# Performance work log

Hardware: AMD Instinct MI355X
Metric: run time of the kernel (lower is better)

## Reference

```python
import jax, jax.numpy as jnp
import numpy as np

B, S, DIM, DA = 64, 4096, 256, 64
NEG = -1e30

def setup_inputs() -> dict:
    key = jax.random.key(0)
    k1, k2, k3, k4 = jax.random.split(key, 4)
    h = jax.random.normal(k1, (B, S, DIM), dtype=jnp.float32)
    mask = jax.random.randint(k2, (B, S), 0, 2).astype(jnp.bool_)
    # xavier_uniform with gain=1.414 as in the torch module
    lim_a = 1.414 * np.sqrt(6.0 / (DIM + DA))
    lim_b = 1.414 * np.sqrt(6.0 / (DA + 1))
    a = jax.random.uniform(k3, (DIM, DA), minval=-lim_a, maxval=lim_a, dtype=jnp.float32)
    b = jax.random.uniform(k4, (DA, 1), minval=-lim_b, maxval=lim_b, dtype=jnp.float32)
    return {"h": h, "mask": mask, "a": a, "b": b}

def reference(h, mask, a, b):
    # e: (B, S) additive-attention logits
    e = jnp.einsum('bsk,ko->bs', jnp.tanh(jnp.einsum('bsd,dk->bsk', h, a)), b)
    e = e + mask.astype(e.dtype) * NEG  # True == padding -> -1e30
    attn = jax.nn.softmax(e, axis=1)    # softmax over seq dim
    # weighted sum over seq: (B, DIM)
    return jnp.einsum('bs,bsd->bd', attn, h)
```

## Files before the change

### kernel.cpp

```cpp
#include <hip/hip_runtime.h>
#include <hip/hip_bf16.h>

#define B_      64
#define S_      4096
#define DIM_    256
#define DA_     64
#define NEG_    (-1e30f)
#define CHUNKS_ 16
#define ROWS_   256
#define TILES_  4
#define LDH_    264
#define PSTR_   258

typedef _Float16 half8 __attribute__((ext_vector_type(8)));
typedef float float4v __attribute__((ext_vector_type(4)));

__global__ __launch_bounds__(256) void prep_kernel(
    const float* __restrict__ a, const void* __restrict__ mask,
    _Float16* __restrict__ at_sw, int* __restrict__ flag)
{
    int idx = blockIdx.x * 256 + threadIdx.x;
    int j    = idx & 7;
    int lane = (idx >> 3) & 63;
    int kbnt = idx >> 9;
    int kb   = kbnt & 7;
    int nt   = kbnt >> 3;
    int d  = kb * 32 + (lane >> 4) * 8 + j;
    int kf = nt * 16 + (lane & 15);
    at_sw[idx] = (_Float16)a[d * DA_ + kf];

    if (blockIdx.x == 0) {
        __shared__ int anynz;
        if (threadIdx.x == 0) anynz = 0;
        __syncthreads();
        const unsigned char* mb = (const unsigned char*)mask;
        int base = threadIdx.x * 4;
        int v = mb[base + 1] | mb[base + 2] | mb[base + 3];
        if (v) atomicOr(&anynz, 1);
        __syncthreads();
        if (threadIdx.x == 0) *flag = (anynz == 0) ? 1 : 0;
    }
}

__global__ __launch_bounds__(256) void fused_kernel(
    const float* __restrict__ h, const _Float16* __restrict__ at_sw,
    const float* __restrict__ bvec, const void* __restrict__ mask,
    const int* __restrict__ flag, float* __restrict__ part)
{
    __shared__ _Float16 hf[64 * LDH_];
    __shared__ float e_l[64];
    __shared__ float w_l[64];
    __shared__ float red[4 * 256];
    __shared__ float m_s, l_s, resc_s;

    const int t = threadIdx.x;
    const int b = blockIdx.x >> 4;
    const int c = blockIdx.x & (CHUNKS_ - 1);
    const int wave = t >> 6;
    const int lane = t & 63;
    const int quad = lane >> 4;
    const int nrow = lane & 15;
    const bool int32enc = (*flag != 0);

    if (t == 0) { m_s = NEG_; l_s = 0.f; }

    const float* hb = h + ((long long)b * S_ + c * ROWS_) * DIM_;
    float bv[4];
    #pragma unroll
    for (int nt = 0; nt < 4; ++nt) bv[nt] = bvec[nt * 16 + nrow];

    const int dbase = (t & 63) * 4;
    float acc0 = 0.f, acc1 = 0.f, acc2 = 0.f, acc3 = 0.f;

    for (int tile = 0; tile < TILES_; ++tile) {
        const float* hsrc = hb + (size_t)tile * 64 * DIM_;
        #pragma unroll
        for (int j = 0; j < 8; ++j) {
            int f2 = t + j * 256;
            int row = f2 >> 5;
            int col = (f2 & 31) * 8;
            const float* src = hsrc + row * DIM_ + col;
            float4 v0 = *(const float4*)(src);
            float4 v1 = *(const float4*)(src + 4);
            union { _Float16 hh[8]; uint4 u; } pk;
            pk.hh[0] = (_Float16)v0.x; pk.hh[1] = (_Float16)v0.y;
            pk.hh[2] = (_Float16)v0.z; pk.hh[3] = (_Float16)v0.w;
            pk.hh[4] = (_Float16)v1.x; pk.hh[5] = (_Float16)v1.y;
            pk.hh[6] = (_Float16)v1.z; pk.hh[7] = (_Float16)v1.w;
            *(uint4*)&hf[row * LDH_ + col] = pk.u;
        }
        __syncthreads();

        float4v accm[4];
        #pragma unroll
        for (int nt = 0; nt < 4; ++nt) accm[nt] = (float4v){0.f, 0.f, 0.f, 0.f};
        const _Float16* hrow = &hf[(wave * 16 + nrow) * LDH_];
        #pragma unroll
        for (int kb = 0; kb < 8; ++kb) {
            half8 af = *(const half8*)(hrow + kb * 32 + quad * 8);
            #pragma unroll
            for (int nt = 0; nt < 4; ++nt) {
                half8 bf = *(const half8*)(at_sw + ((nt * 8 + kb) * 64 + lane) * 8);
                accm[nt] = __builtin_amdgcn_mfma_f32_16x16x32_f16(af, bf, accm[nt], 0, 0, 0);
            }
        }
        #pragma unroll
        for (int r = 0; r < 4; ++r) {
            float p = 0.f;
            #pragma unroll
            for (int nt = 0; nt < 4; ++nt) p += tanhf(accm[nt][r]) * bv[nt];
            p += __shfl_xor(p, 1);
            p += __shfl_xor(p, 2);
            p += __shfl_xor(p, 4);
            p += __shfl_xor(p, 8);
            if (nrow == r) e_l[wave * 16 + quad * 4 + r] = p;
        }
        __syncthreads();

        if (wave == 0) {
            long long mi = (long long)b * S_ + c * ROWS_ + tile * 64 + lane;
            int mv = int32enc ? ((const int*)mask)[mi]
                              : (int)((const unsigned char*)mask)[mi];
            float ev = mv ? NEG_ : e_l[lane];
            float mx = ev;
            #pragma unroll
            for (int off = 32; off >= 1; off >>= 1) mx = fmaxf(mx, __shfl_xor(mx, off));
            float m_old = m_s;
            float m_new = fmaxf(m_old, mx);
            float wv_ = __expf(ev - m_new);
            w_l[lane] = wv_;
            float sm = wv_;
            #pragma unroll
            for (int off = 32; off >= 1; off >>= 1) sm += __shfl_xor(sm, off);
            if (lane == 0) {
                float rs = __expf(m_old - m_new);
                l_s = l_s * rs + sm;
                m_s = m_new;
                resc_s = rs;
            }
        }
        __syncthreads();

        float rs = resc_s;
        acc0 *= rs; acc1 *= rs; acc2 *= rs; acc3 *= rs;
        #pragma unroll 4
        for (int i = 0; i < 16; ++i) {
            int s = i * 4 + wave;
            float ws = w_l[s];
            union { ushort4 u; _Float16 hh[4]; } pk;
            pk.u = *(const ushort4*)((const unsigned short*)&hf[s * LDH_ + dbase]);
            acc0 = fmaf(ws, (float)pk.hh[0], acc0);
            acc1 = fmaf(ws, (float)pk.hh[1], acc1);
            acc2 = fmaf(ws, (float)pk.hh[2], acc2);
            acc3 = fmaf(ws, (float)pk.hh[3], acc3);
        }
        __syncthreads();
    }

    red[wave * 256 + dbase + 0] = acc0;
    red[wave * 256 + dbase + 1] = acc1;
    red[wave * 256 + dbase + 2] = acc2;
    red[wave * 256 + dbase + 3] = acc3;
    __syncthreads();
    float sum = red[t] + red[256 + t] + red[512 + t] + red[768 + t];
    float* pc = part + (size_t)(b * CHUNKS_ + c) * PSTR_;
    pc[2 + t] = sum;
    if (t == 0) { pc[0] = m_s; pc[1] = l_s; }
}

__global__ __launch_bounds__(256) void merge_kernel(
    const float* __restrict__ part, float* __restrict__ out)
{
    const int b = blockIdx.x;
    const int t = threadIdx.x;
    const float* pb = part + (size_t)b * CHUNKS_ * PSTR_;
    float M = NEG_;
    #pragma unroll
    for (int c = 0; c < CHUNKS_; ++c) M = fmaxf(M, pb[c * PSTR_]);
    float L = 0.f, o = 0.f;
    #pragma unroll
    for (int c = 0; c < CHUNKS_; ++c) {
        float sc = __expf(pb[c * PSTR_] - M);
        L += pb[c * PSTR_ + 1] * sc;
        o += pb[c * PSTR_ + 2 + t] * sc;
    }
    out[b * DIM_ + t] = o / L;
}

extern "C" void kernel_launch(void* const* d_in, const int* in_sizes, int n_in,
                              void* d_out, int out_size, void* d_ws, size_t ws_size,
                              hipStream_t stream) {
    const float* h    = (const float*)d_in[0];
    const void*  mask = d_in[1];
    const float* a    = (const float*)d_in[2];
    const float* bvec = (const float*)d_in[3];
    float* out = (float*)d_out;

    char* ws = (char*)d_ws;
    _Float16* at_sw = (_Float16*)ws;
    int* flag       = (int*)(ws + 32768);
    float* part     = (float*)(ws + 36864);

    prep_kernel<<<64, 256, 0, stream>>>(a, mask, at_sw, flag);
    fused_kernel<<<B_ * CHUNKS_, 256, 0, stream>>>(h, at_sw, bvec, mask, flag, part);
    merge_kernel<<<B_, 256, 0, stream>>>(part, out);
}
```

Baseline: 377.2 us.

## Prefetch next h tile into registers, compute softmax per-wave, use fast tanh

Loads the next 64-row tile of h into registers while the current tile is converted and processed, so global-load latency overlaps with compute. The online-softmax bookkeeping is done redundantly in every wave, with weights broadcast through shuffles, which removes one block barrier and the shared-memory state per tile. tanhf is replaced by an exp/reciprocal approximation. In exchange, the prefetch buffer uses 64 extra VGPRs, which may lower occupancy, and the fast tanh gives slightly less accurate results.

```diff
diff --git a/kernel.cpp b/kernel.cpp
--- a/kernel.cpp
+++ b/kernel.cpp
@@ -14,6 +14,11 @@
 
 typedef _Float16 half8 __attribute__((ext_vector_type(8)));
 typedef float float4v __attribute__((ext_vector_type(4)));
+
+static __device__ inline float fast_tanh(float x) {
+    float e = __expf(2.0f * x);
+    return 1.0f - 2.0f * __builtin_amdgcn_rcpf(e + 1.0f);
+}
 
 __global__ __launch_bounds__(256) void prep_kernel(
     const float* __restrict__ a, const void* __restrict__ mask,
@@ -49,9 +54,7 @@
 {
     __shared__ _Float16 hf[64 * LDH_];
     __shared__ float e_l[64];
-    __shared__ float w_l[64];
     __shared__ float red[4 * 256];
-    __shared__ float m_s, l_s, resc_s;
 
     const int t = threadIdx.x;
     const int b = blockIdx.x >> 4;
@@ -62,32 +65,47 @@
     const int nrow = lane & 15;
     const bool int32enc = (*flag != 0);
 
-    if (t == 0) { m_s = NEG_; l_s = 0.f; }
-
     const float* hb = h + ((long long)b * S_ + c * ROWS_) * DIM_;
     float bv[4];
     #pragma unroll
     for (int nt = 0; nt < 4; ++nt) bv[nt] = bvec[nt * 16 + nrow];
 
-    const int dbase = (t & 63) * 4;
+    const int dbase = lane * 4;
     float acc0 = 0.f, acc1 = 0.f, acc2 = 0.f, acc3 = 0.f;
+    float m_w = NEG_, l_w = 0.f;
+
+    float4 pf[16];
+    #pragma unroll
+    for (int j = 0; j < 8; ++j) {
+        int f2 = t + j * 256;
+        const float* src = hb + (f2 >> 5) * DIM_ + (f2 & 31) * 8;
+        pf[2 * j]     = *(const float4*)src;
+        pf[2 * j + 1] = *(const float4*)(src + 4);
+    }
 
     for (int tile = 0; tile < TILES_; ++tile) {
-        const float* hsrc = hb + (size_t)tile * 64 * DIM_;
         #pragma unroll
         for (int j = 0; j < 8; ++j) {
             int f2 = t + j * 256;
             int row = f2 >> 5;
             int col = (f2 & 31) * 8;
-            const float* src = hsrc + row * DIM_ + col;
-            float4 v0 = *(const float4*)(src);
-            float4 v1 = *(const float4*)(src + 4);
+            float4 v0 = pf[2 * j], v1 = pf[2 * j + 1];
             union { _Float16 hh[8]; uint4 u; } pk;
             pk.hh[0] = (_Float16)v0.x; pk.hh[1] = (_Float16)v0.y;
             pk.hh[2] = (_Float16)v0.z; pk.hh[3] = (_Float16)v0.w;
             pk.hh[4] = (_Float16)v1.x; pk.hh[5] = (_Float16)v1.y;
             pk.hh[6] = (_Float16)v1.z; pk.hh[7] = (_Float16)v1.w;
             *(uint4*)&hf[row * LDH_ + col] = pk.u;
+        }
+        if (tile + 1 < TILES_) {
+            const float* hsrc = hb + (size_t)(tile + 1) * 64 * DIM_;
+            #pragma unroll
+            for (int j = 0; j < 8; ++j) {
+                int f2 = t + j * 256;
+                const float* src = hsrc + (f2 >> 5) * DIM_ + (f2 & 31) * 8;
+                pf[2 * j]     = *(const float4*)src;
+                pf[2 * j + 1] = *(const float4*)(src + 4);
+            }
         }
         __syncthreads();
 
@@ -108,7 +126,7 @@
         for (int r = 0; r < 4; ++r) {
             float p = 0.f;
             #pragma unroll
-            for (int nt = 0; nt < 4; ++nt) p += tanhf(accm[nt][r]) * bv[nt];
+            for (int nt = 0; nt < 4; ++nt) p += fast_tanh(accm[nt][r]) * bv[nt];
             p += __shfl_xor(p, 1);
             p += __shfl_xor(p, 2);
             p += __shfl_xor(p, 4);
@@ -117,36 +135,27 @@
         }
         __syncthreads();
 
-        if (wave == 0) {
-            long long mi = (long long)b * S_ + c * ROWS_ + tile * 64 + lane;
-            int mv = int32enc ? ((const int*)mask)[mi]
-                              : (int)((const unsigned char*)mask)[mi];
-            float ev = mv ? NEG_ : e_l[lane];
-            float mx = ev;
-            #pragma unroll
-            for (int off = 32; off >= 1; off >>= 1) mx = fmaxf(mx, __shfl_xor(mx, off));
-            float m_old = m_s;
-            float m_new = fmaxf(m_old, mx);
-            float wv_ = __expf(ev - m_new);
-            w_l[lane] = wv_;
-            float sm = wv_;
-            #pragma unroll
-            for (int off = 32; off >= 1; off >>= 1) sm += __shfl_xor(sm, off);
-            if (lane == 0) {
-                float rs = __expf(m_old - m_new);
-                l_s = l_s * rs + sm;
-                m_s = m_new;
-                resc_s = rs;
-            }
-        }
-        __syncthreads();
-
-        float rs = resc_s;
+        long long mi = (long long)b * S_ + c * ROWS_ + tile * 64 + lane;
+        int mv = int32enc ? ((const int*)mask)[mi]
+                          : (int)((const unsigned char*)mask)[mi];
+        float ev = mv ? NEG_ : e_l[lane];
+        float mx = ev;
+        #pragma unroll
+        for (int off = 32; off >= 1; off >>= 1) mx = fmaxf(mx, __shfl_xor(mx, off));
+        float m_new = fmaxf(m_w, mx);
+        float wv_ = __expf(ev - m_new);
+        float sm = wv_;
+        #pragma unroll
+        for (int off = 32; off >= 1; off >>= 1) sm += __shfl_xor(sm, off);
+        float rs = __expf(m_w - m_new);
+        l_w = l_w * rs + sm;
+        m_w = m_new;
+
         acc0 *= rs; acc1 *= rs; acc2 *= rs; acc3 *= rs;
         #pragma unroll 4
         for (int i = 0; i < 16; ++i) {
             int s = i * 4 + wave;
-            float ws = w_l[s];
+            float ws = __shfl(wv_, s);
             union { ushort4 u; _Float16 hh[4]; } pk;
             pk.u = *(const ushort4*)((const unsigned short*)&hf[s * LDH_ + dbase]);
             acc0 = fmaf(ws, (float)pk.hh[0], acc0);
@@ -165,7 +174,7 @@
     float sum = red[t] + red[256 + t] + red[512 + t] + red[768 + t];
     float* pc = part + (size_t)(b * CHUNKS_ + c) * PSTR_;
     pc[2 + t] = sum;
-    if (t == 0) { pc[0] = m_s; pc[1] = l_s; }
+    if (t == 0) { pc[0] = m_w; pc[1] = l_w; }
 }
 
 __global__ __launch_bounds__(256) void merge_kernel(
```

New measurement: 385.5 us. 2.2% more time.
